# Kernel tuning notes

Hardware: AMD Instinct MI355X
Metric: run time of the kernel (lower is better)

The kernel has to match this reference:

```python
import jax, jax.numpy as jnp
import numpy as np

MASK_RADIUS = 30.0

def _fft_mask(height, width, mode):
    # replicates fft_filter_def: grid over full H rows and rfft half-plane cols
    cht, cwt = height // 2, width // 2
    fy, fx = jnp.meshgrid(jnp.arange(height), jnp.arange(width // 2 + 1), indexing='ij')
    dist = jnp.sqrt((fx - cwt).astype(jnp.float32) ** 2 + (fy - cht).astype(jnp.float32) ** 2)
    if mode == 'high':
        return (dist > MASK_RADIUS).astype(jnp.float32)
    return (dist <= MASK_RADIUS).astype(jnp.float32)


def setup_inputs() -> dict:
    key = jax.random.key(0)
    k1, k2, k3 = jax.random.split(key, 3)
    B, Cin, Cout, H, W, K = 4, 64, 64, 128, 128, 3
    x = jax.random.normal(k1, (B, Cin, H, W), dtype=jnp.float32)
    weight = jax.random.normal(k2, (Cout, Cin, K, K), dtype=jnp.float32) * 0.1
    bias = jax.random.normal(k3, (Cout,), dtype=jnp.float32) * 0.1
    return {"x": x, "weight": weight, "bias": bias}


def reference(x, weight, bias):
    B, Cin, H, W = x.shape
    x = x.astype(jnp.float32)
    # rfft2 of input, then fftshift (as in original; kernel FFT is NOT shifted)
    fft_x = jnp.fft.rfft2(x)                          # [B, Cin, H, W//2+1]
    fft_x = jnp.fft.fftshift(fft_x, axes=(-2, -1))
    kernel_fft = jnp.fft.rfft2(weight, s=(H, W))      # [Cout, Cin, H, W//2+1]
    # high-pass frequency mask (fft_filter == 'high')
    mask = _fft_mask(H, W, 'high')                    # [H, W//2+1]
    fft_x = fft_x * mask
    # per-frequency complex GEMV over in_channels (avoids [B,Cout,Cin,H,Wf] blowup)
    fft_out = jnp.einsum('bihw,oihw->bohw', fft_x, kernel_fft)
    out = jnp.fft.irfft2(fft_out, s=(H, W))           # [B, Cout, H, W]
    return out + bias[None, :, None, None]
```

## Files before the change

### kernel.cpp

```cpp
#include <hip/hip_runtime.h>

#define PI_F 3.14159265358979323846f

#define HH 128
#define WW 128
#define WF 65
#define NB 4
#define NC 64
#define CPLX_PER_IMG (HH * WF)

typedef __attribute__((ext_vector_type(8))) short short8;
typedef __attribute__((ext_vector_type(4))) float f32x4;

__device__ __forceinline__ ushort f2b(float f) {
    unsigned u = __float_as_uint(f);
    u += 0x7fffu + ((u >> 16) & 1u);
    return (ushort)(u >> 16);
}


__global__ __launch_bounds__(256) void k_pre(const float* __restrict__ w,
                                             ushort* __restrict__ A1,
                                             ushort* __restrict__ A2,
                                             ushort* __restrict__ A4,
                                             ushort* __restrict__ A5,
                                             ushort* __restrict__ WvRe,
                                             ushort* __restrict__ WvIm) {
    int idx = blockIdx.x * 256 + threadIdx.x;
    if (idx < 20480) {
        int m = idx >> 7, k = idx & 127;
        int part = m / 80, v = m - part * 80;
        float s, c;
        __sincosf(2.f * PI_F * (float)((v * k) & 127) / 128.f, &s, &c);
        float val = (v < 65) ? (part ? -s : c) : 0.f;
        A1[idx] = f2b(val);
    } else if (idx < 86016) {
        int j = idx - 20480;
        int m = j >> 8, k2 = j & 255;
        int part = m >> 7, u = m & 127;
        int kp = k2 >> 7, h = k2 & 127;
        float s, c;
        __sincosf(2.f * PI_F * (float)((u * h) & 127) / 128.f, &s, &c);
        float val = part == 0 ? (kp == 0 ? c : s) : (kp == 0 ? -s : c);
        A2[j] = f2b(val);
    } else if (idx < 151552) {
        int j = idx - 86016;
        int m = j >> 8, k2 = j & 255;
        int part = m >> 7, h = m & 127;
        int kp = k2 >> 7, u = k2 & 127;
        float s, c;
        __sincosf(2.f * PI_F * (float)((u * h) & 127) / 128.f, &s, &c);
        float val = part == 0 ? (kp == 0 ? c : -s) : (kp == 0 ? s : c);
        A4[j] = f2b(val * (1.f / 128.f));
    } else if (idx < 172032) {
        int j = idx - 151552;
        int x = j / 160, k2 = j - x * 160;
        int part = k2 / 80, v = k2 - part * 80;
        float s, c;
        __sincosf(2.f * PI_F * (float)((v * x) & 127) / 128.f, &s, &c);
        float cv = (v == 0 || v == 64) ? 1.f : 2.f;
        float val = (v < 65) ? (part == 0 ? cv * c : -cv * s) * (1.f / 128.f) : 0.f;
        A5[j] = f2b(val);
    } else {
        int xw = idx - 172032;
        int i = xw & 63;
        int o = (xw >> 6) & 63;
        int pv = xw >> 12;
        int p = pv / WF;
        int v = pv % WF;
        const float* wp = w + ((size_t)o * 64 + i) * 9 + p * 3;
        float re = wp[0], im = 0.f;
#pragma unroll
        for (int q = 1; q <= 2; ++q) {
            int k = (v * q) & 127;
            float s, c;
            __sincosf(-2.f * PI_F * (float)k / 128.f, &s, &c);
            re += wp[q] * c;
            im += wp[q] * s;
        }
        WvRe[xw] = f2b(re);
        WvIm[xw] = f2b(im);
    }
}

#define B1P 136
#define B2P 280
__global__ __launch_bounds__(512) void k_fwd(const float* __restrict__ x,
                                             const ushort* __restrict__ A1,
                                             const ushort* __restrict__ A2,
                                             ushort* __restrict__ XsRe,
                                             ushort* __restrict__ XsIm) {
    __shared__ ushort B1[128 * B1P];
    __shared__ ushort B2[80 * B2P];
    int t = threadIdx.x;
    int img = blockIdx.x;
    const float* gx = x + (size_t)img * 16384;
    for (int c = t; c < 2048; c += 512) {
        int r = c >> 4, sl = c & 15;
        const float* src = gx + r * 128 + sl * 8;
        float4 f0 = *(const float4*)src;
        float4 f1 = *(const float4*)(src + 4);
        short8 v8;
        v8[0] = (short)f2b(f0.x); v8[1] = (short)f2b(f0.y);
        v8[2] = (short)f2b(f0.z); v8[3] = (short)f2b(f0.w);
        v8[4] = (short)f2b(f1.x); v8[5] = (short)f2b(f1.y);
        v8[6] = (short)f2b(f1.z); v8[7] = (short)f2b(f1.w);
        *(short8*)&B1[r * B1P + sl * 8] = v8;
    }
    __syncthreads();
    int lane = t & 63, wave = t >> 6;
    int lrow = lane & 15, lq = lane >> 4;

    {
        f32x4 acc[10];
#pragma unroll
        for (int mt = 0; mt < 10; ++mt) acc[mt] = (f32x4){0.f, 0.f, 0.f, 0.f};
        int hrow = wave * 16 + lrow;
#pragma unroll
        for (int ks = 0; ks < 4; ++ks) {
            short8 b = *(short8*)&B1[hrow * B1P + ks * 32 + lq * 8];
#pragma unroll
            for (int mt = 0; mt < 10; ++mt) {
                short8 a = *(const short8*)&A1[(mt * 16 + lrow) * 128 + ks * 32 + lq * 8];
                acc[mt] = __builtin_amdgcn_mfma_f32_16x16x32_bf16(a, b, acc[mt], 0, 0, 0);
            }
        }
#pragma unroll
        for (int mt = 0; mt < 10; ++mt) {
            int m0 = mt * 16 + lq * 4;
            int part = m0 >= 80;
            int v0 = m0 - part * 80;
#pragma unroll
            for (int e = 0; e < 4; ++e)
                B2[(v0 + e) * B2P + part * 128 + wave * 16 + lrow] = f2b(acc[mt][e]);
        }
    }
    __syncthreads();

    {
        f32x4 acc[5][2];
#pragma unroll
        for (int mt = 0; mt < 5; ++mt)
#pragma unroll
            for (int j = 0; j < 2; ++j) acc[mt][j] = (f32x4){0.f, 0.f, 0.f, 0.f};
#pragma unroll
        for (int ks = 0; ks < 8; ++ks) {
            short8 a[5];
#pragma unroll
            for (int mt = 0; mt < 5; ++mt)
                a[mt] = *(short8*)&B2[(mt * 16 + lrow) * B2P + ks * 32 + lq * 8];
#pragma unroll
            for (int j = 0; j < 2; ++j) {
                int nt = wave * 2 + j;
                short8 b = *(const short8*)&A2[(nt * 16 + lrow) * 256 + ks * 32 + lq * 8];
#pragma unroll
                for (int mt = 0; mt < 5; ++mt)
                    acc[mt][j] = __builtin_amdgcn_mfma_f32_16x16x32_bf16(a[mt], b, acc[mt][j], 0, 0, 0);
            }
        }
#pragma unroll
        for (int j = 0; j < 2; ++j) {
            int nt = wave * 2 + j;
            int part = nt >= 8;
            int u = (nt & 7) * 16 + lrow;
            int u_out = (u + 64) & 127;
            int du = u_out - 64;
            ushort* dimg = (part ? XsIm : XsRe) + (size_t)img * CPLX_PER_IMG;
#pragma unroll
            for (int mt = 0; mt < 5; ++mt)
#pragma unroll
                for (int e = 0; e < 4; ++e) {
                    int v_in = mt * 16 + lq * 4 + e;
                    if (v_in < 65) {
                        int v_out = v_in + 32; if (v_out >= 65) v_out -= 65;
                        int dv = v_out - 64;
                        bool keep = (du * du + dv * dv) > 900;
                        dimg[v_out * 128 + u_out] = keep ? f2b(acc[mt][j][e]) : (ushort)0;
                    }
                }
        }
    }
}

#define AP 72
__global__ __launch_bounds__(256, 2) void k_gemm(const ushort* __restrict__ XsRe,
                                                 const ushort* __restrict__ XsIm,
                                                 const ushort* __restrict__ WvRe,
                                                 const ushort* __restrict__ WvIm,
                                                 ushort* __restrict__ Zre,
                                                 ushort* __restrict__ Zim) {
    __shared__ ushort XTre[128 * AP], XTim[128 * AP];
    __shared__ ushort WSre[64 * AP],  WSim[64 * AP];
    int t = threadIdx.x;
    int v = blockIdx.x >> 2;
    int b = blockIdx.x & 3;
    {
        int u = t & 127, qh = t >> 7;
#pragma unroll
        for (int q8 = 0; q8 < 8; ++q8) {
            int q = qh * 8 + q8;
            ushort re4[4], im4[4];
#pragma unroll
            for (int c = 0; c < 4; ++c) {
                int i = q * 4 + c;
                size_t off = ((size_t)(b * 64 + i) * WF + v) * 128 + u;
                re4[c] = XsRe[off];
                im4[c] = XsIm[off];
            }
            *(ushort4*)&XTre[u * AP + q * 4] = make_ushort4(re4[0], re4[1], re4[2], re4[3]);
            *(ushort4*)&XTim[u * AP + q * 4] = make_ushort4(im4[0], im4[1], im4[2], im4[3]);
        }
    }
    int lane = t & 63, wave = t >> 6;
    int lrow = lane & 15, lq = lane >> 4;
    int u0 = wave * 32;
    f32x4 fRe[8], fIm[8];
#pragma unroll
    for (int m = 0; m < 8; ++m) {
        fRe[m] = (f32x4){0.f, 0.f, 0.f, 0.f};
        fIm[m] = (f32x4){0.f, 0.f, 0.f, 0.f};
    }
    for (int p = 0; p < 3; ++p) {
        if (p) __syncthreads();
        {
            const ushort* gr = WvRe + ((size_t)(p * WF + v)) * 4096;
            const ushort* gi = WvIm + ((size_t)(p * WF + v)) * 4096;
#pragma unroll
            for (int cc = 0; cc < 2; ++cc) {
                int c = t + cc * 256;
                int o = c >> 3, i0 = (c & 7) * 8;
                *(short8*)&WSre[o * AP + i0] = *(const short8*)&gr[c * 8];
                *(short8*)&WSim[o * AP + i0] = *(const short8*)&gi[c * 8];
            }
        }
        __syncthreads();
        f32x4 pRe[8], pIm[8];
#pragma unroll
        for (int m = 0; m < 8; ++m) {
            pRe[m] = (f32x4){0.f, 0.f, 0.f, 0.f};
            pIm[m] = (f32x4){0.f, 0.f, 0.f, 0.f};
        }
#pragma unroll
        for (int ks = 0; ks < 2; ++ks) {
            int kb = ks * 32 + lq * 8;
            short8 br[2], bi[2], bin[2];
#pragma unroll
            for (int ut = 0; ut < 2; ++ut) {
                int u = u0 + ut * 16 + lrow;
                br[ut] = *(const short8*)&XTre[u * AP + kb];
                bi[ut] = *(const short8*)&XTim[u * AP + kb];
                bin[ut] = bi[ut] ^ (short)0x8000;
            }
#pragma unroll
            for (int ot = 0; ot < 4; ++ot) {
                int o = ot * 16 + lrow;
                short8 ar = *(const short8*)&WSre[o * AP + kb];
                short8 ai = *(const short8*)&WSim[o * AP + kb];
#pragma unroll
                for (int ut = 0; ut < 2; ++ut) {
                    int m = ot * 2 + ut;
                    pRe[m] = __builtin_amdgcn_mfma_f32_16x16x32_bf16(ai, bin[ut], pRe[m], 0, 0, 0);
                    pRe[m] = __builtin_amdgcn_mfma_f32_16x16x32_bf16(ar, br[ut],  pRe[m], 0, 0, 0);
                    pIm[m] = __builtin_amdgcn_mfma_f32_16x16x32_bf16(ai, br[ut],  pIm[m], 0, 0, 0);
                    pIm[m] = __builtin_amdgcn_mfma_f32_16x16x32_bf16(ar, bi[ut],  pIm[m], 0, 0, 0);
                }
            }
        }
#pragma unroll
        for (int ut = 0; ut < 2; ++ut) {
            int u = u0 + ut * 16 + lrow;
            float sn, cn;
            __sincosf(-2.f * PI_F * (float)(u * p) / 128.f, &sn, &cn);
#pragma unroll
            for (int ot = 0; ot < 4; ++ot) {
                int m = ot * 2 + ut;
#pragma unroll
                for (int e = 0; e < 4; ++e) {
                    fRe[m][e] += pRe[m][e] * cn - pIm[m][e] * sn;
                    fIm[m][e] += pIm[m][e] * cn + pRe[m][e] * sn;
                }
            }
        }
    }
#pragma unroll
    for (int ot = 0; ot < 4; ++ot)
#pragma unroll
        for (int ut = 0; ut < 2; ++ut) {
            int m = ot * 2 + ut;
            int u = u0 + ut * 16 + lrow;
#pragma unroll
            for (int e = 0; e < 4; ++e) {
                int o = ot * 16 + lq * 4 + e;
                size_t idx = ((size_t)(b * 64 + o) * 65 + v) * 128 + u;
                Zre[idx] = f2b(fRe[m][e]);
                Zim[idx] = f2b(fIm[m][e]);
            }
        }
}

#define B3P 168
__global__ __launch_bounds__(512) void k_inv(const ushort* __restrict__ Zre,
                                             const ushort* __restrict__ Zim,
                                             const ushort* __restrict__ A4,
                                             const ushort* __restrict__ A5,
                                             const float* __restrict__ bias,
                                             float* __restrict__ out) {
    __shared__ ushort B1[80 * B2P];
    __shared__ ushort B2[128 * B3P];
    int t = threadIdx.x;
    int ch = blockIdx.x;
    for (int c = t; c < 2080; c += 512) {
        int r = c >> 5, sl = c & 31;
        const ushort* src = (sl < 16 ? Zre : Zim) + ((size_t)ch * 65 + r) * 128 + (sl & 15) * 8;
        *(short8*)&B1[r * B2P + sl * 8] = *(const short8*)src;
    }
    if (t < 480) {
        int r = 65 + (t >> 5), sl = t & 31;
        short8 z = {0, 0, 0, 0, 0, 0, 0, 0};
        *(short8*)&B1[r * B2P + sl * 8] = z;
    }
    __syncthreads();
    int lane = t & 63, wave = t >> 6;
    int lrow = lane & 15, lq = lane >> 4;

    {
        f32x4 acc[2][5];
#pragma unroll
        for (int m2 = 0; m2 < 2; ++m2)
#pragma unroll
            for (int nt = 0; nt < 5; ++nt) acc[m2][nt] = (f32x4){0.f, 0.f, 0.f, 0.f};
#pragma unroll
        for (int ks = 0; ks < 8; ++ks) {
            short8 b[5];
#pragma unroll
            for (int nt = 0; nt < 5; ++nt)
                b[nt] = *(short8*)&B1[(nt * 16 + lrow) * B2P + ks * 32 + lq * 8];
#pragma unroll
            for (int m2 = 0; m2 < 2; ++m2) {
                int mt = wave * 2 + m2;
                short8 a = *(const short8*)&A4[(mt * 16 + lrow) * 256 + ks * 32 + lq * 8];
#pragma unroll
                for (int nt = 0; nt < 5; ++nt)
                    acc[m2][nt] = __builtin_amdgcn_mfma_f32_16x16x32_bf16(a, b[nt], acc[m2][nt], 0, 0, 0);
            }
        }
#pragma unroll
        for (int m2 = 0; m2 < 2; ++m2) {
            int mt = wave * 2 + m2;
            int part = mt >= 8;
            int h0 = mt * 16 + lq * 4 - part * 128;
#pragma unroll
            for (int nt = 0; nt < 5; ++nt) {
                int v = nt * 16 + lrow;
#pragma unroll
                for (int e = 0; e < 4; ++e)
                    B2[(h0 + e) * B3P + part * 80 + v] = f2b(acc[m2][nt][e]);
            }
        }
    }
    __syncthreads();

    {
        f32x4 acc[8];
#pragma unroll
        for (int nt = 0; nt < 8; ++nt) acc[nt] = (f32x4){0.f, 0.f, 0.f, 0.f};
#pragma unroll
        for (int ks = 0; ks < 5; ++ks) {
            short8 a = *(short8*)&B2[(wave * 16 + lrow) * B3P + ks * 32 + lq * 8];
#pragma unroll
            for (int nt = 0; nt < 8; ++nt) {
                short8 b = *(const short8*)&A5[(nt * 16 + lrow) * 160 + ks * 32 + lq * 8];
                acc[nt] = __builtin_amdgcn_mfma_f32_16x16x32_bf16(a, b, acc[nt], 0, 0, 0);
            }
        }
        float bo = bias[ch & 63];
        float* go = out + (size_t)ch * 16384;
#pragma unroll
        for (int nt = 0; nt < 8; ++nt) {
            int xx = nt * 16 + lrow;
#pragma unroll
            for (int e = 0; e < 4; ++e) {
                int h = wave * 16 + lq * 4 + e;
                go[h * 128 + xx] = acc[nt][e] + bo;
            }
        }
    }
}

extern "C" void kernel_launch(void* const* d_in, const int* in_sizes, int n_in,
                              void* d_out, int out_size, void* d_ws, size_t ws_size,
                              hipStream_t stream) {
    const float* x = (const float*)d_in[0];
    const float* w = (const float*)d_in[1];
    const float* bias = (const float*)d_in[2];
    float* out = (float*)d_out;

    char* ws = (char*)d_ws;
    ushort* A1   = (ushort*)(ws + 0);
    ushort* A2   = (ushort*)(ws + 40960);
    ushort* A4   = (ushort*)(ws + 172032);
    ushort* A5   = (ushort*)(ws + 303104);
    ushort* WvRe = (ushort*)(ws + 344064);
    ushort* WvIm = (ushort*)(ws + 1941504);
    ushort* XsRe = (ushort*)(ws + 12058624);
    ushort* XsIm = (ushort*)(ws + 16318464);
    ushort* Zre  = (ushort*)(ws + 20578304);
    ushort* Zim  = (ushort*)(ws + 24838144);

    k_pre<<<3792, 256, 0, stream>>>(w, A1, A2, A4, A5, WvRe, WvIm);
    k_fwd<<<NB * NC, 512, 0, stream>>>(x, A1, A2, XsRe, XsIm);
    k_gemm<<<WF * NB, 256, 0, stream>>>(XsRe, XsIm, WvRe, WvIm, Zre, Zim);
    k_inv<<<NB * NC, 512, 0, stream>>>(Zre, Zim, A4, A5, bias, out);
}
```

Before: 55.14 us.

## Double threads per block in forward and inverse DFT kernels

k_fwd and k_inv now launch 1024 threads (16 waves) per image instead of 512. The MFMA tiles are redistributed so each wave computes half as many output tiles, which cuts per-wave serial work and register pressure and adds latency hiding within each block. In exchange, operand reuse per wave drops: B2/B1 fragments and A-matrix fragments are reloaded more often across waves, and the larger blocks may limit how many blocks fit per CU.

```diff
diff --git a/kernel.cpp b/kernel.cpp
--- a/kernel.cpp
+++ b/kernel.cpp
@@ -85,17 +85,17 @@
 
 #define B1P 136
 #define B2P 280
-__global__ __launch_bounds__(512) void k_fwd(const float* __restrict__ x,
-                                             const ushort* __restrict__ A1,
-                                             const ushort* __restrict__ A2,
-                                             ushort* __restrict__ XsRe,
-                                             ushort* __restrict__ XsIm) {
+__global__ __launch_bounds__(1024) void k_fwd(const float* __restrict__ x,
+                                              const ushort* __restrict__ A1,
+                                              const ushort* __restrict__ A2,
+                                              ushort* __restrict__ XsRe,
+                                              ushort* __restrict__ XsIm) {
     __shared__ ushort B1[128 * B1P];
     __shared__ ushort B2[80 * B2P];
     int t = threadIdx.x;
     int img = blockIdx.x;
     const float* gx = x + (size_t)img * 16384;
-    for (int c = t; c < 2048; c += 512) {
+    for (int c = t; c < 2048; c += 1024) {
         int r = c >> 4, sl = c & 15;
         const float* src = gx + r * 128 + sl * 8;
         float4 f0 = *(const float4*)src;
@@ -112,73 +112,64 @@
     int lrow = lane & 15, lq = lane >> 4;
 
     {
-        f32x4 acc[10];
-#pragma unroll
-        for (int mt = 0; mt < 10; ++mt) acc[mt] = (f32x4){0.f, 0.f, 0.f, 0.f};
-        int hrow = wave * 16 + lrow;
+        int g = wave >> 3, nt = wave & 7;
+        int hrow = nt * 16 + lrow;
+        f32x4 acc[5];
+#pragma unroll
+        for (int j = 0; j < 5; ++j) acc[j] = (f32x4){0.f, 0.f, 0.f, 0.f};
 #pragma unroll
         for (int ks = 0; ks < 4; ++ks) {
             short8 b = *(short8*)&B1[hrow * B1P + ks * 32 + lq * 8];
 #pragma unroll
-            for (int mt = 0; mt < 10; ++mt) {
+            for (int j = 0; j < 5; ++j) {
+                int mt = g * 5 + j;
                 short8 a = *(const short8*)&A1[(mt * 16 + lrow) * 128 + ks * 32 + lq * 8];
-                acc[mt] = __builtin_amdgcn_mfma_f32_16x16x32_bf16(a, b, acc[mt], 0, 0, 0);
-            }
-        }
-#pragma unroll
-        for (int mt = 0; mt < 10; ++mt) {
-            int m0 = mt * 16 + lq * 4;
+                acc[j] = __builtin_amdgcn_mfma_f32_16x16x32_bf16(a, b, acc[j], 0, 0, 0);
+            }
+        }
+#pragma unroll
+        for (int j = 0; j < 5; ++j) {
+            int m0 = (g * 5 + j) * 16 + lq * 4;
             int part = m0 >= 80;
             int v0 = m0 - part * 80;
 #pragma unroll
             for (int e = 0; e < 4; ++e)
-                B2[(v0 + e) * B2P + part * 128 + wave * 16 + lrow] = f2b(acc[mt][e]);
+                B2[(v0 + e) * B2P + part * 128 + hrow] = f2b(acc[j][e]);
         }
     }
     __syncthreads();
 
     {
-        f32x4 acc[5][2];
+        int nt = wave;
+        f32x4 acc[5];
+#pragma unroll
+        for (int mt = 0; mt < 5; ++mt) acc[mt] = (f32x4){0.f, 0.f, 0.f, 0.f};
+#pragma unroll
+        for (int ks = 0; ks < 8; ++ks) {
+            short8 b = *(const short8*)&A2[(nt * 16 + lrow) * 256 + ks * 32 + lq * 8];
+#pragma unroll
+            for (int mt = 0; mt < 5; ++mt) {
+                short8 a = *(short8*)&B2[(mt * 16 + lrow) * B2P + ks * 32 + lq * 8];
+                acc[mt] = __builtin_amdgcn_mfma_f32_16x16x32_bf16(a, b, acc[mt], 0, 0, 0);
+            }
+        }
+        int part = nt >= 8;
+        int u = (nt & 7) * 16 + lrow;
+        int u_out = (u + 64) & 127;
+        int du = u_out - 64;
+        ushort* dimg = (part ? XsIm : XsRe) + (size_t)img * CPLX_PER_IMG;
 #pragma unroll
         for (int mt = 0; mt < 5; ++mt)
 #pragma unroll
-            for (int j = 0; j < 2; ++j) acc[mt][j] = (f32x4){0.f, 0.f, 0.f, 0.f};
-#pragma unroll
-        for (int ks = 0; ks < 8; ++ks) {
-            short8 a[5];
-#pragma unroll
-            for (int mt = 0; mt < 5; ++mt)
-                a[mt] = *(short8*)&B2[(mt * 16 + lrow) * B2P + ks * 32 + lq * 8];
-#pragma unroll
-            for (int j = 0; j < 2; ++j) {
-                int nt = wave * 2 + j;
-                short8 b = *(const short8*)&A2[(nt * 16 + lrow) * 256 + ks * 32 + lq * 8];
-#pragma unroll
-                for (int mt = 0; mt < 5; ++mt)
-                    acc[mt][j] = __builtin_amdgcn_mfma_f32_16x16x32_bf16(a[mt], b, acc[mt][j], 0, 0, 0);
-            }
-        }
-#pragma unroll
-        for (int j = 0; j < 2; ++j) {
-            int nt = wave * 2 + j;
-            int part = nt >= 8;
-            int u = (nt & 7) * 16 + lrow;
-            int u_out = (u + 64) & 127;
-            int du = u_out - 64;
-            ushort* dimg = (part ? XsIm : XsRe) + (size_t)img * CPLX_PER_IMG;
-#pragma unroll
-            for (int mt = 0; mt < 5; ++mt)
-#pragma unroll
-                for (int e = 0; e < 4; ++e) {
-                    int v_in = mt * 16 + lq * 4 + e;
-                    if (v_in < 65) {
-                        int v_out = v_in + 32; if (v_out >= 65) v_out -= 65;
-                        int dv = v_out - 64;
-                        bool keep = (du * du + dv * dv) > 900;
-                        dimg[v_out * 128 + u_out] = keep ? f2b(acc[mt][j][e]) : (ushort)0;
-                    }
+            for (int e = 0; e < 4; ++e) {
+                int v_in = mt * 16 + lq * 4 + e;
+                if (v_in < 65) {
+                    int v_out = v_in + 32; if (v_out >= 65) v_out -= 65;
+                    int dv = v_out - 64;
+                    bool keep = (du * du + dv * dv) > 900;
+                    dimg[v_out * 128 + u_out] = keep ? f2b(acc[mt][e]) : (ushort)0;
                 }
-        }
+            }
     }
 }
 
@@ -299,17 +290,17 @@
 }
 
 #define B3P 168
-__global__ __launch_bounds__(512) void k_inv(const ushort* __restrict__ Zre,
-                                             const ushort* __restrict__ Zim,
-                                             const ushort* __restrict__ A4,
-                                             const ushort* __restrict__ A5,
-                                             const float* __restrict__ bias,
-                                             float* __restrict__ out) {
+__global__ __launch_bounds__(1024) void k_inv(const ushort* __restrict__ Zre,
+                                              const ushort* __restrict__ Zim,
+                                              const ushort* __restrict__ A4,
+                                              const ushort* __restrict__ A5,
+                                              const float* __restrict__ bias,
+                                              float* __restrict__ out) {
     __shared__ ushort B1[80 * B2P];
     __shared__ ushort B2[128 * B3P];
     int t = threadIdx.x;
     int ch = blockIdx.x;
-    for (int c = t; c < 2080; c += 512) {
+    for (int c = t; c < 2080; c += 1024) {
         int r = c >> 5, sl = c & 31;
         const ushort* src = (sl < 16 ? Zre : Zim) + ((size_t)ch * 65 + r) * 128 + (sl & 15) * 8;
         *(short8*)&B1[r * B2P + sl * 8] = *(const short8*)src;
@@ -324,64 +315,55 @@
     int lrow = lane & 15, lq = lane >> 4;
 
     {
-        f32x4 acc[2][5];
-#pragma unroll
-        for (int m2 = 0; m2 < 2; ++m2)
-#pragma unroll
-            for (int nt = 0; nt < 5; ++nt) acc[m2][nt] = (f32x4){0.f, 0.f, 0.f, 0.f};
+        int mt = wave;
+        f32x4 acc[5];
+#pragma unroll
+        for (int nt = 0; nt < 5; ++nt) acc[nt] = (f32x4){0.f, 0.f, 0.f, 0.f};
 #pragma unroll
         for (int ks = 0; ks < 8; ++ks) {
-            short8 b[5];
-#pragma unroll
-            for (int nt = 0; nt < 5; ++nt)
-                b[nt] = *(short8*)&B1[(nt * 16 + lrow) * B2P + ks * 32 + lq * 8];
-#pragma unroll
-            for (int m2 = 0; m2 < 2; ++m2) {
-                int mt = wave * 2 + m2;
-                short8 a = *(const short8*)&A4[(mt * 16 + lrow) * 256 + ks * 32 + lq * 8];
-#pragma unroll
-                for (int nt = 0; nt < 5; ++nt)
-                    acc[m2][nt] = __builtin_amdgcn_mfma_f32_16x16x32_bf16(a, b[nt], acc[m2][nt], 0, 0, 0);
-            }
-        }
-#pragma unroll
-        for (int m2 = 0; m2 < 2; ++m2) {
-            int mt = wave * 2 + m2;
-            int part = mt >= 8;
-            int h0 = mt * 16 + lq * 4 - part * 128;
+            short8 a = *(const short8*)&A4[(mt * 16 + lrow) * 256 + ks * 32 + lq * 8];
 #pragma unroll
             for (int nt = 0; nt < 5; ++nt) {
-                int v = nt * 16 + lrow;
-#pragma unroll
-                for (int e = 0; e < 4; ++e)
-                    B2[(h0 + e) * B3P + part * 80 + v] = f2b(acc[m2][nt][e]);
-            }
+                short8 b = *(short8*)&B1[(nt * 16 + lrow) * B2P + ks * 32 + lq * 8];
+                acc[nt] = __builtin_amdgcn_mfma_f32_16x16x32_bf16(a, b, acc[nt], 0, 0, 0);
+            }
+        }
+        int part = mt >= 8;
+        int h0 = mt * 16 + lq * 4 - part * 128;
+#pragma unroll
+        for (int nt = 0; nt < 5; ++nt) {
+            int v = nt * 16 + lrow;
+#pragma unroll
+            for (int e = 0; e < 4; ++e)
+                B2[(h0 + e) * B3P + part * 80 + v] = f2b(acc[nt][e]);
         }
     }
     __syncthreads();
 
     {
-        f32x4 acc[8];
-#pragma unroll
-        for (int nt = 0; nt < 8; ++nt) acc[nt] = (f32x4){0.f, 0.f, 0.f, 0.f};
+        int mt = wave & 7, nh = wave >> 3;
+        f32x4 acc[4];
+#pragma unroll
+        for (int jn = 0; jn < 4; ++jn) acc[jn] = (f32x4){0.f, 0.f, 0.f, 0.f};
 #pragma unroll
         for (int ks = 0; ks < 5; ++ks) {
-            short8 a = *(short8*)&B2[(wave * 16 + lrow) * B3P + ks * 32 + lq * 8];
-#pragma unroll
-            for (int nt = 0; nt < 8; ++nt) {
+            short8 a = *(short8*)&B2[(mt * 16 + lrow) * B3P + ks * 32 + lq * 8];
+#pragma unroll
+            for (int jn = 0; jn < 4; ++jn) {
+                int nt = nh * 4 + jn;
                 short8 b = *(const short8*)&A5[(nt * 16 + lrow) * 160 + ks * 32 + lq * 8];
-                acc[nt] = __builtin_amdgcn_mfma_f32_16x16x32_bf16(a, b, acc[nt], 0, 0, 0);
+                acc[jn] = __builtin_amdgcn_mfma_f32_16x16x32_bf16(a, b, acc[jn], 0, 0, 0);
             }
         }
         float bo = bias[ch & 63];
         float* go = out + (size_t)ch * 16384;
 #pragma unroll
-        for (int nt = 0; nt < 8; ++nt) {
-            int xx = nt * 16 + lrow;
+        for (int jn = 0; jn < 4; ++jn) {
+            int xx = (nh * 4 + jn) * 16 + lrow;
 #pragma unroll
             for (int e = 0; e < 4; ++e) {
-                int h = wave * 16 + lq * 4 + e;
-                go[h * 128 + xx] = acc[nt][e] + bo;
+                int h = mt * 16 + lq * 4 + e;
+                go[h * 128 + xx] = acc[jn][e] + bo;
             }
         }
     }
@@ -408,7 +390,7 @@
     ushort* Zim  = (ushort*)(ws + 24838144);
 
     k_pre<<<3792, 256, 0, stream>>>(w, A1, A2, A4, A5, WvRe, WvIm);
-    k_fwd<<<NB * NC, 512, 0, stream>>>(x, A1, A2, XsRe, XsIm);
+    k_fwd<<<NB * NC, 1024, 0, stream>>>(x, A1, A2, XsRe, XsIm);
     k_gemm<<<WF * NB, 256, 0, stream>>>(XsRe, XsIm, WvRe, WvIm, Zre, Zim);
-    k_inv<<<NB * NC, 512, 0, stream>>>(Zre, Zim, A4, A5, bias, out);
-}
+    k_inv<<<NB * NC, 1024, 0, stream>>>(Zre, Zim, A4, A5, bias, out);
+}
```

Measured after the change: 54.21 us. About the same (-1.7%).
